# Optimization experiments

Measured on AMD Instinct MI355X. Metric: run time of the kernel, lower is better.

Reference implementation:

```python
import jax, jax.numpy as jnp
import numpy as np

KY, KX = 3, 3  # kernel_size from init_kwargs


def setup_inputs() -> dict:
    key = jax.random.key(0)
    x = jax.random.normal(key, (8, 64, 256, 256), dtype=jnp.float32)
    return {"x": x}


def reference(x):
    # NMS: mask = x > max over 3x3 replicate-padded neighborhood EXCLUDING center.
    # Note: the torch conv kernel zeroes the center row, so the center output
    # channel is all zeros and the max implicitly includes 0 — we replicate that
    # by initializing the running max to zeros.
    ky, kx = KY, KX
    py, px = (ky - 1) // 2, (kx - 1) // 2
    H, W = x.shape[-2], x.shape[-1]
    xp = jnp.pad(x, ((0, 0), (0, 0), (py, py), (px, px)), mode='edge')  # replicate pad
    numel = ky * kx
    center = numel // 2
    max_non_center = jnp.zeros_like(x)  # zeroed-center channel participates in max
    for i in range(numel):  # fixed small kernel window, unrolled (8 shifts)
        if i == center:
            continue
        dy, dx = divmod(i, kx)
        max_non_center = jnp.maximum(max_non_center, xp[..., dy:dy + H, dx:dx + W])
    mask = x > max_non_center
    return x * mask.astype(x.dtype)
```

## Files before the change

### kernel.cpp

```cpp
#include <hip/hip_runtime.h>


#define NMS_H 256
#define NMS_W 256
#define PLANE (NMS_H * NMS_W)
#define GROUPS_PER_PLANE (NMS_H / 4)
#define NGROUPS (512 * GROUPS_PER_PLANE)

typedef float f4_t __attribute__((ext_vector_type(4)));

struct HV {
    float4 h;
    float4 lr;
};

__device__ __forceinline__ HV rowmax(const float4 v, const int tx) {
    float l = __shfl_up(v.w, 1, 64);
    float r = __shfl_down(v.x, 1, 64);
    if (tx == 0)  l = v.x;
    if (tx == 63) r = v.w;
    HV o;
    o.h.x = fmaxf(l,   fmaxf(v.x, v.y));
    o.h.y = fmaxf(v.x, fmaxf(v.y, v.z));
    o.h.z = fmaxf(v.y, fmaxf(v.z, v.w));
    o.h.w = fmaxf(v.z, fmaxf(v.w, r));
    o.lr.x = fmaxf(l,   v.y);
    o.lr.y = fmaxf(v.x, v.z);
    o.lr.z = fmaxf(v.y, v.w);
    o.lr.w = fmaxf(v.z, r);
    return o;
}

__global__ __launch_bounds__(256) void nms2d_kernel(const float* __restrict__ x,
                                                    float* __restrict__ out) {
    const int tx    = threadIdx.x;
    const int col4  = tx * 4;
    const int wave  = blockIdx.x * blockDim.y + threadIdx.y;
    const int nwave = gridDim.x * blockDim.y;

    for (int g = wave; g < NGROUPS; g += nwave) {
        const int plane_idx = g >> 6;
        const int r0        = (g & 63) * 4;
        const float* pl = x   + (size_t)plane_idx * PLANE;
        float*       op = out + (size_t)plane_idx * PLANE;

        float4 v[6];
        #pragma unroll
        for (int i = 0; i < 6; ++i) {
            const int r = min(max(r0 + i - 1, 0), NMS_H - 1);
            v[i] = *reinterpret_cast<const float4*>(pl + r * NMS_W + col4);
        }

        HV m[6];
        #pragma unroll
        for (int i = 0; i < 6; ++i) m[i] = rowmax(v[i], tx);

        #pragma unroll
        for (int i = 0; i < 4; ++i) {
            const float4 ctr = v[i + 1];
            const float4 ha = m[i].h, hb = m[i + 2].h, lc = m[i + 1].lr;
            f4_t o;
            float mm;
            mm = fmaxf(0.0f, fmaxf(fmaxf(ha.x, hb.x), lc.x)); o.x = (ctr.x > mm) ? ctr.x : 0.0f;
            mm = fmaxf(0.0f, fmaxf(fmaxf(ha.y, hb.y), lc.y)); o.y = (ctr.y > mm) ? ctr.y : 0.0f;
            mm = fmaxf(0.0f, fmaxf(fmaxf(ha.z, hb.z), lc.z)); o.z = (ctr.z > mm) ? ctr.z : 0.0f;
            mm = fmaxf(0.0f, fmaxf(fmaxf(ha.w, hb.w), lc.w)); o.w = (ctr.w > mm) ? ctr.w : 0.0f;
            __builtin_nontemporal_store(o, reinterpret_cast<f4_t*>(op + (r0 + i) * NMS_W + col4));
        }
    }
}

extern "C" void kernel_launch(void* const* d_in, const int* in_sizes, int n_in,
                              void* d_out, int out_size, void* d_ws, size_t ws_size,
                              hipStream_t stream) {
    const float* x = (const float*)d_in[0];
    float* out = (float*)d_out;

    dim3 block(64, 4);
    dim3 grid(2048);
    nms2d_kernel<<<grid, block, 0, stream>>>(x, out);
}
```

Baseline: 227.6 us.

## Stage 16-row strips in LDS via direct global-to-LDS loads

Replaces the persistent grid-stride loop, where each wave loaded six overlapping rows from global memory, with one block per 16-row strip. The strip plus its halo rows goes into shared memory through global_load_lds, so halo rows are read from global memory 18/16 times instead of 6/4. The grid grows to 8192 blocks, which adds a barrier and some launch and scheduling overhead. Nontemporal stores become plain stores.

```diff
diff --git a/kernel.cpp b/kernel.cpp
--- a/kernel.cpp
+++ b/kernel.cpp
@@ -4,8 +4,8 @@
 #define NMS_H 256
 #define NMS_W 256
 #define PLANE (NMS_H * NMS_W)
-#define GROUPS_PER_PLANE (NMS_H / 4)
-#define NGROUPS (512 * GROUPS_PER_PLANE)
+#define STRIP 16
+#define LROWS (STRIP + 2)
 
 typedef float f4_t __attribute__((ext_vector_type(4)));
 
@@ -33,40 +33,50 @@
 
 __global__ __launch_bounds__(256) void nms2d_kernel(const float* __restrict__ x,
                                                     float* __restrict__ out) {
-    const int tx    = threadIdx.x;
-    const int col4  = tx * 4;
-    const int wave  = blockIdx.x * blockDim.y + threadIdx.y;
-    const int nwave = gridDim.x * blockDim.y;
+    __shared__ float lds[LROWS * NMS_W];
 
-    for (int g = wave; g < NGROUPS; g += nwave) {
-        const int plane_idx = g >> 6;
-        const int r0        = (g & 63) * 4;
-        const float* pl = x   + (size_t)plane_idx * PLANE;
-        float*       op = out + (size_t)plane_idx * PLANE;
+    const int tx   = threadIdx.x;
+    const int ty   = threadIdx.y;
+    const int col4 = tx * 4;
+    const int blk  = blockIdx.x;
+    const int plane_idx = blk >> 4;
+    const int r0        = (blk & 15) * STRIP;
 
-        float4 v[6];
-        #pragma unroll
-        for (int i = 0; i < 6; ++i) {
-            const int r = min(max(r0 + i - 1, 0), NMS_H - 1);
-            v[i] = *reinterpret_cast<const float4*>(pl + r * NMS_W + col4);
-        }
+    const float* pl = x   + (size_t)plane_idx * PLANE;
+    float*       op = out + (size_t)plane_idx * PLANE;
 
-        HV m[6];
-        #pragma unroll
-        for (int i = 0; i < 6; ++i) m[i] = rowmax(v[i], tx);
+    #pragma unroll
+    for (int j = ty; j < LROWS; j += 4) {
+        const int r = min(max(r0 + j - 1, 0), NMS_H - 1);
+        const __attribute__((address_space(1))) float* g =
+            (const __attribute__((address_space(1))) float*)(pl + r * NMS_W + col4);
+        __attribute__((address_space(3))) float* l =
+            (__attribute__((address_space(3))) float*)(&lds[j * NMS_W]);
+        __builtin_amdgcn_global_load_lds(g, l, 16, 0, 0);
+    }
+    __syncthreads();
 
-        #pragma unroll
-        for (int i = 0; i < 4; ++i) {
-            const float4 ctr = v[i + 1];
-            const float4 ha = m[i].h, hb = m[i + 2].h, lc = m[i + 1].lr;
-            f4_t o;
-            float mm;
-            mm = fmaxf(0.0f, fmaxf(fmaxf(ha.x, hb.x), lc.x)); o.x = (ctr.x > mm) ? ctr.x : 0.0f;
-            mm = fmaxf(0.0f, fmaxf(fmaxf(ha.y, hb.y), lc.y)); o.y = (ctr.y > mm) ? ctr.y : 0.0f;
-            mm = fmaxf(0.0f, fmaxf(fmaxf(ha.z, hb.z), lc.z)); o.z = (ctr.z > mm) ? ctr.z : 0.0f;
-            mm = fmaxf(0.0f, fmaxf(fmaxf(ha.w, hb.w), lc.w)); o.w = (ctr.w > mm) ? ctr.w : 0.0f;
-            __builtin_nontemporal_store(o, reinterpret_cast<f4_t*>(op + (r0 + i) * NMS_W + col4));
-        }
+    const int base = ty * 4;
+    float4 v[6];
+    #pragma unroll
+    for (int i = 0; i < 6; ++i)
+        v[i] = *reinterpret_cast<const float4*>(&lds[(base + i) * NMS_W + col4]);
+
+    HV m[6];
+    #pragma unroll
+    for (int i = 0; i < 6; ++i) m[i] = rowmax(v[i], tx);
+
+    #pragma unroll
+    for (int i = 0; i < 4; ++i) {
+        const float4 ctr = v[i + 1];
+        const float4 ha = m[i].h, hb = m[i + 2].h, lc = m[i + 1].lr;
+        f4_t o;
+        float mm;
+        mm = fmaxf(0.0f, fmaxf(fmaxf(ha.x, hb.x), lc.x)); o.x = (ctr.x > mm) ? ctr.x : 0.0f;
+        mm = fmaxf(0.0f, fmaxf(fmaxf(ha.y, hb.y), lc.y)); o.y = (ctr.y > mm) ? ctr.y : 0.0f;
+        mm = fmaxf(0.0f, fmaxf(fmaxf(ha.z, hb.z), lc.z)); o.z = (ctr.z > mm) ? ctr.z : 0.0f;
+        mm = fmaxf(0.0f, fmaxf(fmaxf(ha.w, hb.w), lc.w)); o.w = (ctr.w > mm) ? ctr.w : 0.0f;
+        *reinterpret_cast<f4_t*>(op + (r0 + base + i) * NMS_W + col4) = o;
     }
 }
 
@@ -77,6 +87,6 @@
     float* out = (float*)d_out;
 
     dim3 block(64, 4);
-    dim3 grid(2048);
+    dim3 grid(8192);
     nms2d_kernel<<<grid, block, 0, stream>>>(x, out);
 }
```

Result: no change. 228.7 us (+0.5%).
